# Optimization experiments

Measured on AMD Instinct MI355X. Metric: run time of the kernel, lower is better.

## Reference

```python
import jax, jax.numpy as jnp
import numpy as np

B, H, WD = 4, 1440, 1440      # batch, BEV grid (sparse_shape)
N, C, NB = 200000, 32, 3      # active voxels, channels, num basic blocks
EPS = 1e-3                    # BatchNorm1d eps in the module


def setup_inputs() -> dict:
    key = jax.random.key(0)
    ks = jax.random.split(key, 10)
    feats = jax.random.normal(ks[0], (N, C), jnp.float32)
    coords_b = jax.random.randint(ks[1], (N,), 0, B, dtype=jnp.int32)
    coords_y = jax.random.randint(ks[2], (N,), 0, H, dtype=jnp.int32)
    coords_x = jax.random.randint(ks[3], (N,), 0, WD, dtype=jnp.int32)
    # [block, conv(2), tap(3x3=9), Cin, Cout]; fan-in scaled init
    Wk = jax.random.normal(ks[4], (NB, 2, 9, C, C), jnp.float32) / np.sqrt(9 * C)
    bias = 0.01 * jax.random.normal(ks[5], (NB, 2, C), jnp.float32)
    gamma = 1.0 + 0.1 * jax.random.normal(ks[6], (NB, 2, C), jnp.float32)
    beta = 0.1 * jax.random.normal(ks[7], (NB, 2, C), jnp.float32)
    mean = 0.1 * jax.random.normal(ks[8], (NB, 2, C), jnp.float32)
    var = jax.random.uniform(ks[9], (NB, 2, C), jnp.float32, 0.5, 1.5)
    return dict(feats=feats, Wk=Wk, bias=bias, gamma=gamma, beta=beta,
                mean=mean, var=var, coords_b=coords_b, coords_y=coords_y,
                coords_x=coords_x)


def _build_rulebook(coords_b, coords_y, coords_x):
    # Dense hash: grid cell -> voxel row id (-1 if empty). Shared by all
    # submanifold convs in the stage (same indice_key in the original).
    idx_map = jnp.full((B, H, WD), -1, jnp.int32)
    idx_map = idx_map.at[coords_b, coords_y, coords_x].set(
        jnp.arange(N, dtype=jnp.int32))
    offs = jnp.array([(dy, dx) for dy in (-1, 0, 1) for dx in (-1, 0, 1)],
                     jnp.int32)                      # [9,2]
    ny = coords_y[None, :] + offs[:, 0:1]            # [9,N]
    nx = coords_x[None, :] + offs[:, 1:2]
    inb = (ny >= 0) & (ny < H) & (nx >= 0) & (nx < WD)
    nyc = jnp.clip(ny, 0, H - 1)
    nxc = jnp.clip(nx, 0, WD - 1)
    nidx = idx_map[jnp.broadcast_to(coords_b[None, :], (9, N)), nyc, nxc]
    mask = inb & (nidx >= 0)
    nidx = jnp.where(mask, nidx, 0)                  # safe gather index
    return nidx, mask[..., None].astype(jnp.float32)


def reference(feats, Wk, bias, gamma, beta, mean, var,
              coords_b, coords_y, coords_x):
    nidx, maskf = _build_rulebook(coords_b, coords_y, coords_x)

    def subm(x, w, b):
        # gather-GEMM-scatter submanifold 3x3 conv on active sites only
        g = x[nidx] * maskf                          # [9,N,Cin]
        return jnp.einsum('knc,kco->no', g, w) + b   # [N,Cout]

    def bn(x, g_, b_, m_, v_):
        return (x - m_) * jax.lax.rsqrt(v_ + EPS) * g_ + b_

    h = feats
    for i in range(NB):  # SparseBasicBlock stack (fixed small layer count)
        identity = h
        o = jax.nn.relu(bn(subm(h, Wk[i, 0], bias[i, 0]),
                           gamma[i, 0], beta[i, 0], mean[i, 0], var[i, 0]))
        o = bn(subm(o, Wk[i, 1], bias[i, 1]),
               gamma[i, 1], beta[i, 1], mean[i, 1], var[i, 1])
        h = jax.nn.relu(o + identity)
    return h
```

## Files before the change

### kernel.cpp

```cpp
#include <hip/hip_runtime.h>

#define NB_ 3
#define CB 4
#define CH 1440
#define CW 1440
#define NC 32
#define EPSV 1e-3f

typedef __attribute__((ext_vector_type(8))) short bf16x8;
typedef __attribute__((ext_vector_type(16))) float f32x16;

union U16 { uint4 u; bf16x8 v; };

__device__ __forceinline__ unsigned pk2(float a, float b) {
    unsigned ua = __float_as_uint(a), ub = __float_as_uint(b);
    ua += 0x7fffu + ((ua >> 16) & 1u);
    ub += 0x7fffu + ((ub >> 16) & 1u);
    return (ua >> 16) | (ub & 0xffff0000u);
}
__device__ __forceinline__ unsigned short f2b(float a) {
    unsigned u = __float_as_uint(a);
    u += 0x7fffu + ((u >> 16) & 1u);
    return (unsigned short)(u >> 16);
}
__device__ __forceinline__ float b2f(unsigned short s) {
    return __uint_as_float(((unsigned)s) << 16);
}

__global__ __launch_bounds__(256) void k_clear(
    const int* __restrict__ cb, const int* __restrict__ cy, const int* __restrict__ cx,
    int* __restrict__ idx_map, int n)
{
    int i = blockIdx.x * blockDim.x + threadIdx.x;
    if (i >= n) return;
    int b = cb[i], y = cy[i], x = cx[i];
    #pragma unroll
    for (int dy = -1; dy <= 1; ++dy) {
        int yy = y + dy;
        if (yy < 0 || yy >= CH) continue;
        #pragma unroll
        for (int dx = -1; dx <= 1; ++dx) {
            int xx = x + dx;
            if (xx < 0 || xx >= CW) continue;
            idx_map[((long)b * CH + yy) * CW + xx] = -1;
        }
    }
}

__global__ __launch_bounds__(256) void k_build_map(
    const int* __restrict__ cb, const int* __restrict__ cy, const int* __restrict__ cx,
    int* __restrict__ idx_map, int n)
{
    int i = blockIdx.x * blockDim.x + threadIdx.x;
    if (i < n) {
        long cell = ((long)cb[i] * CH + cy[i]) * CW + cx[i];
        atomicMax(&idx_map[cell], i);
    }
}

__global__ __launch_bounds__(256) void k_rulebook(
    const int* __restrict__ cb, const int* __restrict__ cy, const int* __restrict__ cx,
    const int* __restrict__ idx_map, int* __restrict__ roff, int n)
{
    int i = blockIdx.x * blockDim.x + threadIdx.x;
    if (i >= n) return;
    int b = cb[i], y = cy[i], x = cx[i];
    roff[4 * n + i] = idx_map[((long)b * CH + y) * CW + x] * 64;
    #pragma unroll
    for (int k = 0; k < 9; ++k) {
        if (k == 4) continue;
        int dy = k / 3 - 1, dx = k % 3 - 1;
        int ny = y + dy, nx = x + dx;
        int nb = -1;
        if (ny >= 0 && ny < CH && nx >= 0 && nx < CW)
            nb = idx_map[((long)b * CH + ny) * CW + nx];
        roff[k * n + i] = (nb >= 0) ? nb * 64 : -1;
    }
}

__global__ __launch_bounds__(256) void k_cvt(
    const float* __restrict__ f, unsigned short* __restrict__ b, int n32)
{
    int i = (blockIdx.x * 256 + threadIdx.x) * 8;
    if (i + 8 <= n32) {
        float4 a0 = *(const float4*)(f + i);
        float4 a1 = *(const float4*)(f + i + 4);
        uint4 r;
        r.x = pk2(a0.x, a0.y); r.y = pk2(a0.z, a0.w);
        r.z = pk2(a1.x, a1.y); r.w = pk2(a1.z, a1.w);
        *(uint4*)(b + i) = r;
    }
}

__global__ __launch_bounds__(256) void k_wcvt(
    const float* __restrict__ Wk, uint4* __restrict__ Bfg,
    unsigned short* __restrict__ z0, unsigned short* __restrict__ z1,
    unsigned short* __restrict__ z2)
{
    if (blockIdx.x == 0 && threadIdx.x < 12) {
        uint4 z = make_uint4(0, 0, 0, 0);
        int tt = threadIdx.x;
        if (tt < 4)       ((uint4*)z0)[tt] = z;
        else if (tt < 8)  ((uint4*)z1)[tt - 4] = z;
        else              ((uint4*)z2)[tt - 8] = z;
    }
    int t = blockIdx.x * 256 + threadIdx.x;
    if (t >= 6 * 9 * 2 * 64) return;
    int l = t & 63, h = (t >> 6) & 1;
    int rest = t >> 7;
    int k = rest % 9, layer = rest / 9;
    int o = l & 31;
    int c0 = h * 16 + 8 * (l >> 5);
    const float* wp = Wk + (size_t)layer * 9216 + k * 1024 + o;
    uint4 r;
    r.x = pk2(wp[(c0 + 0) * 32], wp[(c0 + 1) * 32]);
    r.y = pk2(wp[(c0 + 2) * 32], wp[(c0 + 3) * 32]);
    r.z = pk2(wp[(c0 + 4) * 32], wp[(c0 + 5) * 32]);
    r.w = pk2(wp[(c0 + 6) * 32], wp[(c0 + 7) * 32]);
    Bfg[t] = r;
}

template<bool ADD_ID, bool F32OUT>
__global__ __launch_bounds__(256, 6) void k_conv(
    const unsigned short* __restrict__ in,
    const unsigned short* __restrict__ idn,
    void* __restrict__ outv,
    const uint4* __restrict__ Bf,
    const float* __restrict__ bias,
    const float* __restrict__ gamma, const float* __restrict__ beta,
    const float* __restrict__ mean, const float* __restrict__ var,
    const int* __restrict__ roff, int n)
{
    int l = threadIdx.x & 63, wv = threadIdx.x >> 6;
    int q = l & 31, h5 = l >> 5;

    int ntile = (n + 31) >> 5;
    int tile = blockIdx.x * 4 + wv;
    if (tile >= ntile) return;

    float sc = gamma[q] * rsqrtf(var[q] + EPSV);
    float sh = (bias[q] - mean[q]) * sc + beta[q];

    const int zoff = n * 64;
    const char* inB = (const char*)in;

    int p0 = tile << 5;
    int pr = p0 + q;
    bool rowok = pr < n;
    int prc = rowok ? pr : n - 1;

    int rk[9];
    #pragma unroll
    for (int k = 0; k < 9; ++k) rk[k] = roff[(size_t)k * n + prc];

    f32x16 acc = {0.f,0.f,0.f,0.f,0.f,0.f,0.f,0.f,0.f,0.f,0.f,0.f,0.f,0.f,0.f,0.f};

    #pragma unroll
    for (int g = 0; g < 3; ++g) {
        bool act[3];
        U16 a0[3], a1[3];
        #pragma unroll
        for (int j = 0; j < 3; ++j) {
            int k = g * 3 + j;
            act[j] = __any(rk[k] >= 0);
            if (act[j]) {
                int off = (rowok && rk[k] >= 0) ? rk[k] : zoff;
                const char* ap = inB + off + h5 * 16;
                a0[j].u = *(const uint4*)(ap);
                a1[j].u = *(const uint4*)(ap + 32);
            }
        }
        #pragma unroll
        for (int j = 0; j < 3; ++j) {
            int k = g * 3 + j;
            if (act[j]) {
                U16 b0, b1;
                b0.u = Bf[(k * 2 + 0) * 64 + l];
                b1.u = Bf[(k * 2 + 1) * 64 + l];
                acc = __builtin_amdgcn_mfma_f32_32x32x16_bf16(a0[j].v, b0.v, acc, 0, 0, 0);
                acc = __builtin_amdgcn_mfma_f32_32x32x16_bf16(a1[j].v, b1.v, acc, 0, 0, 0);
            }
        }
    }

    #pragma unroll
    for (int r = 0; r < 16; ++r) {
        int p = p0 + (r & 3) + 8 * (r >> 2) + 4 * h5;
        if (p < n) {
            float y = acc[r] * sc + sh;
            if (ADD_ID) y += b2f(idn[(size_t)p * 32 + q]);
            y = fmaxf(y, 0.f);
            if (F32OUT) ((float*)outv)[(size_t)p * 32 + q] = y;
            else ((unsigned short*)outv)[(size_t)p * 32 + q] = f2b(y);
        }
    }
}

extern "C" void kernel_launch(void* const* d_in, const int* in_sizes, int n_in,
                              void* d_out, int out_size, void* d_ws, size_t ws_size,
                              hipStream_t stream)
{
    const float* feats = (const float*)d_in[0];
    const float* Wk    = (const float*)d_in[1];
    const float* bias  = (const float*)d_in[2];
    const float* gamma = (const float*)d_in[3];
    const float* beta  = (const float*)d_in[4];
    const float* mean  = (const float*)d_in[5];
    const float* var   = (const float*)d_in[6];
    const int* cb = (const int*)d_in[7];
    const int* cy = (const int*)d_in[8];
    const int* cx = (const int*)d_in[9];
    float* out = (float*)d_out;
    int n = in_sizes[0] / NC;

    char* ws = (char*)d_ws;
    int*            idx_map = (int*)(ws + 0);
    int*            roff    = (int*)(ws + 33177600);
    uint4*          Bfg     = (uint4*)(ws + 40377600);
    unsigned short* xbf     = (unsigned short*)(ws + 40488192);
    unsigned short* tmpbf   = (unsigned short*)(ws + 53288256);
    unsigned short* hb      = (unsigned short*)(ws + 66088320);

    int blocks = (n + 255) / 256;
    k_clear<<<blocks, 256, 0, stream>>>(cb, cy, cx, idx_map, n);
    k_build_map<<<blocks, 256, 0, stream>>>(cb, cy, cx, idx_map, n);
    k_rulebook<<<blocks, 256, 0, stream>>>(cb, cy, cx, idx_map, roff, n);
    k_cvt<<<(n * NC / 8 + 255) / 256, 256, 0, stream>>>(feats, xbf, n * NC);
    k_wcvt<<<(6 * 9 * 2 * 64 + 255) / 256, 256, 0, stream>>>(
        Wk, Bfg, xbf + (size_t)n * 32, tmpbf + (size_t)n * 32, hb + (size_t)n * 32);

    const int ntile = (n + 31) / 32;
    const int G = (ntile + 3) / 4;
    const int BSZ = 9 * 2 * 64;

    k_conv<false, false><<<G, 256, 0, stream>>>(xbf, nullptr, tmpbf,
        Bfg + 0 * BSZ, bias + 0,  gamma + 0,  beta + 0,  mean + 0,  var + 0,  roff, n);
    k_conv<true,  false><<<G, 256, 0, stream>>>(tmpbf, xbf, hb,
        Bfg + 1 * BSZ, bias + 32, gamma + 32, beta + 32, mean + 32, var + 32, roff, n);
    k_conv<false, false><<<G, 256, 0, stream>>>(hb, nullptr, tmpbf,
        Bfg + 2 * BSZ, bias + 64, gamma + 64, beta + 64, mean + 64, var + 64, roff, n);
    k_conv<true,  false><<<G, 256, 0, stream>>>(tmpbf, hb, xbf,
        Bfg + 3 * BSZ, bias + 96, gamma + 96, beta + 96, mean + 96, var + 96, roff, n);
    k_conv<false, false><<<G, 256, 0, stream>>>(xbf, nullptr, tmpbf,
        Bfg + 4 * BSZ, bias + 128, gamma + 128, beta + 128, mean + 128, var + 128, roff, n);
    k_conv<true,  true><<<G, 256, 0, stream>>>(tmpbf, xbf, out,
        Bfg + 5 * BSZ, bias + 160, gamma + 160, beta + 160, mean + 160, var + 160, roff, n);
}
```

Before: 135.9 us.

## Replace dense grid index map with open-addressing hash table and merge prep kernels

The dense 33MB idx_map with scattered clear/build is replaced by a 4MB linear-probing hash table (Fibonacci hash, 64-bit key|index entries inserted via CAS, with atomicMax for duplicate keys). A memset clears the table instead of the scattered 9-neighbour clear. Rulebook construction, feature bf16 conversion and weight packing are merged into one kernel launch. Launch count drops and the working set of the lookup structure shrinks to fit better in cache. In exchange, each neighbour lookup may probe several slots, and the table is sized to stay under roughly 40% load.

```diff
diff --git a/kernel.cpp b/kernel.cpp
--- a/kernel.cpp
+++ b/kernel.cpp
@@ -7,6 +7,10 @@
 #define NC 32
 #define EPSV 1e-3f
 
+#define HBITS 19
+#define HSIZE (1u << HBITS)
+#define HMASK (HSIZE - 1)
+
 typedef __attribute__((ext_vector_type(8))) short bf16x8;
 typedef __attribute__((ext_vector_type(16))) float f32x16;
 
@@ -27,97 +31,101 @@
     return __uint_as_float(((unsigned)s) << 16);
 }
 
-__global__ __launch_bounds__(256) void k_clear(
+__device__ __forceinline__ unsigned hash_of(unsigned key) {
+    return (key * 2654435761u) >> (32 - HBITS);
+}
+
+__global__ __launch_bounds__(256) void k_hinsert(
     const int* __restrict__ cb, const int* __restrict__ cy, const int* __restrict__ cx,
-    int* __restrict__ idx_map, int n)
+    unsigned long long* __restrict__ tab, int n)
 {
     int i = blockIdx.x * blockDim.x + threadIdx.x;
     if (i >= n) return;
-    int b = cb[i], y = cy[i], x = cx[i];
-    #pragma unroll
-    for (int dy = -1; dy <= 1; ++dy) {
-        int yy = y + dy;
-        if (yy < 0 || yy >= CH) continue;
-        #pragma unroll
-        for (int dx = -1; dx <= 1; ++dx) {
-            int xx = x + dx;
-            if (xx < 0 || xx >= CW) continue;
-            idx_map[((long)b * CH + yy) * CW + xx] = -1;
-        }
-    }
-}
-
-__global__ __launch_bounds__(256) void k_build_map(
+    unsigned key = ((unsigned)cb[i] * CH + (unsigned)cy[i]) * CW + (unsigned)cx[i];
+    unsigned long long pk = (((unsigned long long)(key + 1)) << 32) | (unsigned)i;
+    unsigned h = hash_of(key);
+    for (;;) {
+        unsigned long long old = atomicCAS(&tab[h], 0ull, pk);
+        if (old == 0ull) break;
+        if ((unsigned)(old >> 32) == key + 1) { atomicMax(&tab[h], pk); break; }
+        h = (h + 1) & HMASK;
+    }
+}
+
+__device__ __forceinline__ int hquery(const unsigned long long* __restrict__ tab,
+                                      unsigned key)
+{
+    unsigned h = hash_of(key);
+    for (;;) {
+        unsigned long long v = tab[h];
+        if (v == 0ull) return -1;
+        if ((unsigned)(v >> 32) == key + 1) return (int)(v & 0xffffffffu);
+        h = (h + 1) & HMASK;
+    }
+}
+
+__global__ __launch_bounds__(256) void k_prep(
     const int* __restrict__ cb, const int* __restrict__ cy, const int* __restrict__ cx,
-    int* __restrict__ idx_map, int n)
-{
-    int i = blockIdx.x * blockDim.x + threadIdx.x;
-    if (i < n) {
-        long cell = ((long)cb[i] * CH + cy[i]) * CW + cx[i];
-        atomicMax(&idx_map[cell], i);
-    }
-}
-
-__global__ __launch_bounds__(256) void k_rulebook(
-    const int* __restrict__ cb, const int* __restrict__ cy, const int* __restrict__ cx,
-    const int* __restrict__ idx_map, int* __restrict__ roff, int n)
-{
-    int i = blockIdx.x * blockDim.x + threadIdx.x;
-    if (i >= n) return;
-    int b = cb[i], y = cy[i], x = cx[i];
-    roff[4 * n + i] = idx_map[((long)b * CH + y) * CW + x] * 64;
-    #pragma unroll
-    for (int k = 0; k < 9; ++k) {
-        if (k == 4) continue;
-        int dy = k / 3 - 1, dx = k % 3 - 1;
-        int ny = y + dy, nx = x + dx;
-        int nb = -1;
-        if (ny >= 0 && ny < CH && nx >= 0 && nx < CW)
-            nb = idx_map[((long)b * CH + ny) * CW + nx];
-        roff[k * n + i] = (nb >= 0) ? nb * 64 : -1;
-    }
-}
-
-__global__ __launch_bounds__(256) void k_cvt(
-    const float* __restrict__ f, unsigned short* __restrict__ b, int n32)
-{
-    int i = (blockIdx.x * 256 + threadIdx.x) * 8;
-    if (i + 8 <= n32) {
-        float4 a0 = *(const float4*)(f + i);
-        float4 a1 = *(const float4*)(f + i + 4);
-        uint4 r;
-        r.x = pk2(a0.x, a0.y); r.y = pk2(a0.z, a0.w);
-        r.z = pk2(a1.x, a1.y); r.w = pk2(a1.z, a1.w);
-        *(uint4*)(b + i) = r;
-    }
-}
-
-__global__ __launch_bounds__(256) void k_wcvt(
+    const unsigned long long* __restrict__ tab, int* __restrict__ roff,
+    const float* __restrict__ feats, unsigned short* __restrict__ xbf,
     const float* __restrict__ Wk, uint4* __restrict__ Bfg,
     unsigned short* __restrict__ z0, unsigned short* __restrict__ z1,
-    unsigned short* __restrict__ z2)
-{
-    if (blockIdx.x == 0 && threadIdx.x < 12) {
-        uint4 z = make_uint4(0, 0, 0, 0);
-        int tt = threadIdx.x;
-        if (tt < 4)       ((uint4*)z0)[tt] = z;
-        else if (tt < 8)  ((uint4*)z1)[tt - 4] = z;
-        else              ((uint4*)z2)[tt - 8] = z;
-    }
-    int t = blockIdx.x * 256 + threadIdx.x;
-    if (t >= 6 * 9 * 2 * 64) return;
-    int l = t & 63, h = (t >> 6) & 1;
-    int rest = t >> 7;
-    int k = rest % 9, layer = rest / 9;
-    int o = l & 31;
-    int c0 = h * 16 + 8 * (l >> 5);
-    const float* wp = Wk + (size_t)layer * 9216 + k * 1024 + o;
-    uint4 r;
-    r.x = pk2(wp[(c0 + 0) * 32], wp[(c0 + 1) * 32]);
-    r.y = pk2(wp[(c0 + 2) * 32], wp[(c0 + 3) * 32]);
-    r.z = pk2(wp[(c0 + 4) * 32], wp[(c0 + 5) * 32]);
-    r.w = pk2(wp[(c0 + 6) * 32], wp[(c0 + 7) * 32]);
-    Bfg[t] = r;
+    unsigned short* __restrict__ z2, int n)
+{
+    int RB = (n + 255) >> 8;
+    int CVT = ((n * NC / 8) + 255) >> 8;
+    int bx = blockIdx.x;
+
+    if (bx < RB) {
+        int i = bx * 256 + threadIdx.x;
+        if (i >= n) return;
+        int b = cb[i], y = cy[i], x = cx[i];
+        unsigned key = ((unsigned)b * CH + (unsigned)y) * CW + (unsigned)x;
+        roff[4 * n + i] = hquery(tab, key) * 64;
+        #pragma unroll
+        for (int k = 0; k < 9; ++k) {
+            if (k == 4) continue;
+            int dy = k / 3 - 1, dx = k % 3 - 1;
+            int ny = y + dy, nx = x + dx;
+            int nb = -1;
+            if (ny >= 0 && ny < CH && nx >= 0 && nx < CW)
+                nb = hquery(tab, key + dy * CW + dx);
+            roff[k * n + i] = (nb >= 0) ? nb * 64 : -1;
+        }
+    } else if (bx < RB + CVT) {
+        int i = ((bx - RB) * 256 + threadIdx.x) * 8;
+        if (i + 8 <= n * NC) {
+            float4 a0 = *(const float4*)(feats + i);
+            float4 a1 = *(const float4*)(feats + i + 4);
+            uint4 r;
+            r.x = pk2(a0.x, a0.y); r.y = pk2(a0.z, a0.w);
+            r.z = pk2(a1.x, a1.y); r.w = pk2(a1.z, a1.w);
+            *(uint4*)(xbf + i) = r;
+        }
+    } else {
+        int wb = bx - RB - CVT;
+        if (wb == 0 && threadIdx.x < 12) {
+            uint4 z = make_uint4(0, 0, 0, 0);
+            int tt = threadIdx.x;
+            if (tt < 4)       ((uint4*)z0)[tt] = z;
+            else if (tt < 8)  ((uint4*)z1)[tt - 4] = z;
+            else              ((uint4*)z2)[tt - 8] = z;
+        }
+        int t = wb * 256 + threadIdx.x;
+        if (t >= 6 * 9 * 2 * 64) return;
+        int l = t & 63, h = (t >> 6) & 1;
+        int rest = t >> 7;
+        int k = rest % 9, layer = rest / 9;
+        int o = l & 31;
+        int c0 = h * 16 + 8 * (l >> 5);
+        const float* wp = Wk + (size_t)layer * 9216 + k * 1024 + o;
+        uint4 r;
+        r.x = pk2(wp[(c0 + 0) * 32], wp[(c0 + 1) * 32]);
+        r.y = pk2(wp[(c0 + 2) * 32], wp[(c0 + 3) * 32]);
+        r.z = pk2(wp[(c0 + 4) * 32], wp[(c0 + 5) * 32]);
+        r.w = pk2(wp[(c0 + 6) * 32], wp[(c0 + 7) * 32]);
+        Bfg[t] = r;
+    }
 }
 
 template<bool ADD_ID, bool F32OUT>
@@ -214,20 +222,21 @@
     int n = in_sizes[0] / NC;
 
     char* ws = (char*)d_ws;
-    int*            idx_map = (int*)(ws + 0);
-    int*            roff    = (int*)(ws + 33177600);
-    uint4*          Bfg     = (uint4*)(ws + 40377600);
-    unsigned short* xbf     = (unsigned short*)(ws + 40488192);
-    unsigned short* tmpbf   = (unsigned short*)(ws + 53288256);
-    unsigned short* hb      = (unsigned short*)(ws + 66088320);
-
-    int blocks = (n + 255) / 256;
-    k_clear<<<blocks, 256, 0, stream>>>(cb, cy, cx, idx_map, n);
-    k_build_map<<<blocks, 256, 0, stream>>>(cb, cy, cx, idx_map, n);
-    k_rulebook<<<blocks, 256, 0, stream>>>(cb, cy, cx, idx_map, roff, n);
-    k_cvt<<<(n * NC / 8 + 255) / 256, 256, 0, stream>>>(feats, xbf, n * NC);
-    k_wcvt<<<(6 * 9 * 2 * 64 + 255) / 256, 256, 0, stream>>>(
-        Wk, Bfg, xbf + (size_t)n * 32, tmpbf + (size_t)n * 32, hb + (size_t)n * 32);
+    unsigned long long* tab  = (unsigned long long*)(ws + 0);
+    int*            roff     = (int*)(ws + 4194304);
+    uint4*          Bfg      = (uint4*)(ws + 11394304);
+    unsigned short* xbf      = (unsigned short*)(ws + 11504896);
+    unsigned short* tmpbf    = (unsigned short*)(ws + 24304960);
+    unsigned short* hb       = (unsigned short*)(ws + 37105024);
+
+    hipMemsetAsync(tab, 0, (size_t)HSIZE * 8, stream);
+
+    int RB  = (n + 255) / 256;
+    int CVT = ((n * NC / 8) + 255) / 256;
+    k_hinsert<<<RB, 256, 0, stream>>>(cb, cy, cx, tab, n);
+    k_prep<<<RB + CVT + 27, 256, 0, stream>>>(
+        cb, cy, cx, tab, roff, feats, xbf, Wk, Bfg,
+        xbf + (size_t)n * 32, tmpbf + (size_t)n * 32, hb + (size_t)n * 32, n);
 
     const int ntile = (n + 31) / 32;
     const int G = (ntile + 3) / 4;
```

New measurement: 141.5 us. 4.1% more time.
